# Performance work log

Measured on AMD Instinct MI355X. Metric: run time of the kernel, lower is better.

Reference implementation:

```python
import jax, jax.numpy as jnp
import numpy as np

N_HEADS = 16
N_KV_HEADS = 4
HEAD_DIM = 128
ROPE_THETA = 1000000.0

def setup_inputs() -> dict:
    key = jax.random.key(0)
    ks = jax.random.split(key, 5)
    B, T, D = 2, 2048, 2048
    s = 1.0 / np.sqrt(D)
    return {
        'x':  jax.random.normal(ks[0], (B, T, D), dtype=jnp.float32),
        'wq': jax.random.normal(ks[1], (D, N_HEADS * HEAD_DIM), dtype=jnp.float32) * s,
        'wk': jax.random.normal(ks[2], (D, N_KV_HEADS * HEAD_DIM), dtype=jnp.float32) * s,
        'wv': jax.random.normal(ks[3], (D, N_KV_HEADS * HEAD_DIM), dtype=jnp.float32) * s,
        'wo': jax.random.normal(ks[4], (N_HEADS * HEAD_DIM, D), dtype=jnp.float32) * s,
    }

def _rope_cos_sin(T, dtype):
    # build_rope_cache: inv_freq over half the head dim, cos/sin of shape [T, HEAD_DIM]
    half = HEAD_DIM // 2
    inv_freq = 1.0 / (ROPE_THETA ** (jnp.arange(0, half, dtype=jnp.float32) * 2.0 / HEAD_DIM))
    ang = jnp.arange(T, dtype=jnp.float32)[:, None] * inv_freq[None, :]  # [T, half]
    ang = jnp.concatenate([ang, ang], axis=-1)  # [T, HEAD_DIM]
    return jnp.cos(ang).astype(dtype), jnp.sin(ang).astype(dtype)

def _rotate_half(u):
    u1, u2 = jnp.split(u, 2, axis=-1)
    return jnp.concatenate([-u2, u1], axis=-1)

def _apply_rotary(h, cos, sin):
    # h: [B, H, T, hd]; cos/sin: [T, hd]
    return h * cos[None, None, :, :] + _rotate_half(h) * sin[None, None, :, :]

def _attention(x, wq, wk, wv, wo):
    B, T, D = x.shape
    dtype = x.dtype
    scale = HEAD_DIM ** -0.5
    # QKV projection + split heads -> [B, H, T, hd]
    qh = (x @ wq).reshape(B, T, N_HEADS, HEAD_DIM).transpose(0, 2, 1, 3)
    kh = (x @ wk).reshape(B, T, N_KV_HEADS, HEAD_DIM).transpose(0, 2, 1, 3)
    vh = (x @ wv).reshape(B, T, N_KV_HEADS, HEAD_DIM).transpose(0, 2, 1, 3)
    # RoPE
    cos, sin = _rope_cos_sin(T, dtype)
    qh = _apply_rotary(qh, cos, sin)
    kh = _apply_rotary(kh, cos, sin)
    # GQA: repeat kv heads
    rep = N_HEADS // N_KV_HEADS
    kh = jnp.repeat(kh, rep, axis=1)
    vh = jnp.repeat(vh, rep, axis=1)
    # eager attention: full score matrix [B, H, T, T]
    scores = jnp.einsum('bhtd,bhsd->bhts', qh, kh) * scale
    causal = jnp.tril(jnp.ones((T, T), dtype=bool))
    neg = jnp.asarray(jnp.finfo(jnp.float32).min, dtype=jnp.float32)
    scores = jnp.where(causal[None, None, :, :], scores.astype(jnp.float32), neg)
    probs = jax.nn.softmax(scores, axis=-1).astype(dtype)
    out = jnp.einsum('bhts,bhsd->bhtd', probs, vh)
    y = out.transpose(0, 2, 1, 3).reshape(B, T, N_HEADS * HEAD_DIM)  # merge heads
    return y @ wo

def reference(x, wq, wk, wv, wo):
    return _attention(x, wq, wk, wv, wo)
```

## Files before the change

kernel.cpp:

```cpp
#include <hip/hip_runtime.h>


#define T_SZ 2048
#define D_SZ 2048
#define BT   4096

typedef __attribute__((ext_vector_type(8))) short bf16x8;
typedef __attribute__((ext_vector_type(4))) float f32x4;

__device__ __forceinline__ unsigned short f2b(float f) {
  unsigned u = __float_as_uint(f);
  u = (u + 0x7fffu + ((u >> 16) & 1u)) >> 16;
  return (unsigned short)u;
}
__device__ __forceinline__ float b2f(unsigned short h) {
  return __uint_as_float(((unsigned)h) << 16);
}

#if __has_builtin(__builtin_amdgcn_exp2f)
__device__ __forceinline__ float exp2_fast(float x) { return __builtin_amdgcn_exp2f(x); }
#else
__device__ __forceinline__ float exp2_fast(float x) {
  float r; asm("v_exp_f32 %0, %1" : "=v"(r) : "v"(x)); return r;
}
#endif

__device__ __forceinline__ void async_ld16(const void* g, void* l) {
  __builtin_amdgcn_global_load_lds(
      (const __attribute__((address_space(1))) void*)g,
      (__attribute__((address_space(3))) void*)l, 16, 0, 0);
}

union Pack8 { unsigned short us[8]; uint4 v; };

__global__ __launch_bounds__(256) void prep(
    const float* __restrict__ x, unsigned short* __restrict__ xb,
    const float* __restrict__ wq, const float* __restrict__ wk,
    const float* __restrict__ wv, const float* __restrict__ wo,
    unsigned short* __restrict__ qkvT, unsigned short* __restrict__ woT) {
  __shared__ float tile[64][68];
  int bid = blockIdx.x, t = threadIdx.x;
  if (bid < 8192) {
    int i = (bid * 256 + t) * 4;
    float4 v = *(const float4*)(x + i);
    ushort4 o;
    o.x = f2b(v.x); o.y = f2b(v.y); o.z = f2b(v.z); o.w = f2b(v.w);
    *(ushort4*)(xb + i) = o;
    return;
  }
  int rem = bid - 8192;
  int bx = rem % 80, ky = rem / 80;
  const float* W; unsigned short* WT; int N, nb;
  if (bx < 32)      { W = wq; WT = qkvT;                       N = 2048; nb = bx; }
  else if (bx < 40) { W = wk; WT = qkvT + (size_t)2048 * 2048; N = 512;  nb = bx - 32; }
  else if (bx < 48) { W = wv; WT = qkvT + (size_t)2560 * 2048; N = 512;  nb = bx - 40; }
  else              { W = wo; WT = woT;                        N = 2048; nb = bx - 48; }
  const int K = 2048;
  int n0 = nb * 64, k0 = ky * 64;
#pragma unroll
  for (int i = 0; i < 4; i++) {
    int c = t + 256 * i;
    int r = c >> 4, cc = c & 15;
    float4 v = *(const float4*)(W + (size_t)(k0 + r) * N + n0 + cc * 4);
    tile[r][cc * 4 + 0] = v.x; tile[r][cc * 4 + 1] = v.y;
    tile[r][cc * 4 + 2] = v.z; tile[r][cc * 4 + 3] = v.w;
  }
  __syncthreads();
#pragma unroll
  for (int i = 0; i < 2; i++) {
    int c = t + 256 * i;
    int n = c >> 3, kc = c & 7;
    Pack8 p;
#pragma unroll
    for (int j = 0; j < 8; j++) p.us[j] = f2b(tile[kc * 8 + j][n]);
    *(uint4*)(WT + (size_t)(n0 + n) * K + k0 + kc * 8) = p.v;
  }
}

template <int OUT_BF16>
__global__ __launch_bounds__(256) void gemm_bt(
    const unsigned short* __restrict__ A, const unsigned short* __restrict__ Bt,
    void* __restrict__ C, int M, int N, int K) {
  __shared__ unsigned short As[2][128 * 32];
  __shared__ unsigned short Bs[2][128 * 32];
  int t = threadIdx.x;
  int lane = t & 63, wave = t >> 6;
  int lin = blockIdx.y * gridDim.x + blockIdx.x;
  int cpx = (gridDim.x * gridDim.y) >> 3;
  int swz = (lin & 7) * cpx + (lin >> 3);
  int bx = swz % gridDim.x, by = swz / gridDim.x;
  int m0 = by * 128, n0 = bx * 128;
  int wm = (wave >> 1) * 64, wn = (wave & 1) * 64;
  int fr = lane & 15, fq = lane >> 4;

  int srow = wave * 32 + (lane >> 2);
  int scol = (lane & 3) * 8;
  const unsigned short* Ag = A + (size_t)(m0 + srow) * K + scol;
  const unsigned short* Bg = Bt + (size_t)(n0 + srow) * K + scol;

  auto stage = [&](int k0_, int bf) {
#pragma unroll
    for (int j = 0; j < 2; j++) {
      async_ld16(Ag + (size_t)j * 16 * K + k0_, &As[bf][wave * 1024 + j * 512]);
      async_ld16(Bg + (size_t)j * 16 * K + k0_, &Bs[bf][wave * 1024 + j * 512]);
    }
  };

  f32x4 acc[4][4];
#pragma unroll
  for (int mi = 0; mi < 4; mi++)
#pragma unroll
    for (int ni = 0; ni < 4; ni++) acc[mi][ni] = (f32x4){0.f, 0.f, 0.f, 0.f};

  stage(0, 0);
  int cur = 0;
  for (int k0 = 0; k0 < K; k0 += 32) {
    if (k0 + 32 < K) {
      stage(k0 + 32, cur ^ 1);
      asm volatile("s_waitcnt vmcnt(4)" ::: "memory");
    } else {
      asm volatile("s_waitcnt vmcnt(0)" ::: "memory");
    }
    __builtin_amdgcn_s_barrier();
    asm volatile("" ::: "memory");
    bf16x8 a[4], b[4];
#pragma unroll
    for (int mi = 0; mi < 4; mi++)
      a[mi] = *(const bf16x8*)(&As[cur][(wm + 16 * mi + fr) * 32 + fq * 8]);
#pragma unroll
    for (int ni = 0; ni < 4; ni++)
      b[ni] = *(const bf16x8*)(&Bs[cur][(wn + 16 * ni + fr) * 32 + fq * 8]);
#pragma unroll
    for (int mi = 0; mi < 4; mi++)
#pragma unroll
      for (int ni = 0; ni < 4; ni++)
        acc[mi][ni] = __builtin_amdgcn_mfma_f32_16x16x32_bf16(
            a[mi], b[ni], acc[mi][ni], 0, 0, 0);
    asm volatile("s_waitcnt lgkmcnt(0)" ::: "memory");
    __builtin_amdgcn_s_barrier();
    asm volatile("" ::: "memory");
    cur ^= 1;
  }
#pragma unroll
  for (int mi = 0; mi < 4; mi++)
#pragma unroll
    for (int ni = 0; ni < 4; ni++)
#pragma unroll
      for (int r = 0; r < 4; r++) {
        int row = m0 + wm + 16 * mi + fq * 4 + r;
        int col = n0 + wn + 16 * ni + fr;
        float v = acc[mi][ni][r];
        if (OUT_BF16)
          ((unsigned short*)C)[(size_t)row * N + col] = f2b(v);
        else
          ((float*)C)[(size_t)row * N + col] = v;
      }
}

__global__ __launch_bounds__(256) void prep2(
    unsigned short* __restrict__ Kx ,
    const unsigned short* __restrict__ V ,
    unsigned short* __restrict__ VT) {
  __shared__ unsigned short tile[64][72];
  int bid = blockIdx.x, t = threadIdx.x;
  if (bid < 4096) {
    int p = bid * 256 + t;
    int d = p & 63;
    int h = (p >> 6) & 3;
    int row = p >> 8;
    int tpos = row & (T_SZ - 1);
    size_t base = (size_t)row * 3072 + h * 128 + d;
    float u1 = b2f(Kx[base]), u2 = b2f(Kx[base + 64]);
    float inv = expf(-(float)d * 0.21586735246819178f);
    float ang = (float)tpos * inv;
    float c = cosf(ang), s = sinf(ang);
    Kx[base]      = f2b(u1 * c - u2 * s);
    Kx[base + 64] = f2b(u2 * c + u1 * s);
    return;
  }
  int c0 = bid - 4096;
  int t0 = (c0 & 31) * 64;
  int n0 = ((c0 >> 5) & 1) * 64;
  int bk = c0 >> 6;
  int b = bk >> 2, kvh = bk & 3;
#pragma unroll
  for (int i = 0; i < 2; i++) {
    int c = t + 256 * i;
    int r = c >> 3, cc = c & 7;
    *(uint4*)&tile[r][cc * 8] = *(const uint4*)(
        V + (size_t)(b * T_SZ + t0 + r) * 3072 + kvh * 128 + n0 + cc * 8);
  }
  __syncthreads();
#pragma unroll
  for (int i = 0; i < 2; i++) {
    int c = t + 256 * i;
    int n = c >> 3, tc = c & 7;
    Pack8 p;
#pragma unroll
    for (int j = 0; j < 8; j++) p.us[j] = tile[tc * 8 + j][n];
    *(uint4*)(VT + ((size_t)bk * 128 + n0 + n) * T_SZ + t0 + tc * 8) = p.v;
  }
}

__global__ __launch_bounds__(512) void attn(
    const unsigned short* __restrict__ Q,
    const unsigned short* __restrict__ KV,
    const unsigned short* __restrict__ VT,
    unsigned short* __restrict__ O) {
  __shared__ unsigned short Ks[2][64 * 128];
  __shared__ unsigned short Vt[128 * 64];
  __shared__ unsigned short Ps[8][16 * 76];
  int qt = blockIdx.z ? blockIdx.x : 15 - blockIdx.x;
  int h = blockIdx.y, b = blockIdx.z;
  int kvh = h >> 2;
  int t = threadIdx.x, lane = t & 63, w = t >> 6;
  int fr = lane & 15, fq = lane >> 4;
  int rsw = fr & 7;

  bf16x8 qf[4];
#pragma unroll
  for (int kk = 0; kk < 4; kk++)
    qf[kk] = *(const bf16x8*)(
        Q + (size_t)(b * T_SZ + qt * 128 + w * 16 + fr) * 3072 +
        h * 128 + kk * 32 + fq * 8);

  const unsigned short* Kg = KV + (size_t)b * T_SZ * 3072 + kvh * 128;
  const unsigned short* Vg = VT + (size_t)(b * 4 + kvh) * 128 * T_SZ;

  int k_lr = lane >> 4, k_ls = lane & 15;
  int v_lr = lane >> 3, v_ls = lane & 7;

  auto stage_k = [&](int kt_, int bf) {
#pragma unroll
    for (int j = 0; j < 2; j++) {
      int row = w * 8 + j * 4 + k_lr;
      async_ld16(Kg + (size_t)(kt_ * 64 + row) * 3072 + ((k_ls ^ (row & 7)) << 3),
                 &Ks[bf][(w * 8 + j * 4) * 128]);
    }
  };
  auto stage_v = [&](int kt_) {
#pragma unroll
    for (int j = 0; j < 2; j++) {
      int row = w * 16 + j * 8 + v_lr;
      async_ld16(Vg + (size_t)row * T_SZ + kt_ * 64 + ((v_ls ^ (row & 7)) << 3),
                 &Vt[(w * 16 + j * 8) * 64]);
    }
  };

  stage_k(0, 0);
  stage_v(0);

  {
    const float QSCL = 0.08838834764831845f * 1.4426950408889634f;
    float tposf = (float)(qt * 128 + w * 16 + fr);
#pragma unroll
    for (int kk = 0; kk < 2; kk++)
#pragma unroll
      for (int j = 0; j < 8; j++) {
        int d = kk * 32 + (fq << 3) + j;
        float u1 = b2f((unsigned short)qf[kk][j]);
        float u2 = b2f((unsigned short)qf[kk + 2][j]);
        float inv = __expf(-(float)d * 0.21586735246819178f);
        float ang = tposf * inv, c, s;
        __sincosf(ang, &s, &c);
        qf[kk][j]     = (short)f2b((u1 * c - u2 * s) * QSCL);
        qf[kk + 2][j] = (short)f2b((u2 * c + u1 * s) * QSCL);
      }
  }

  f32x4 o[8];
#pragma unroll
  for (int i = 0; i < 8; i++) o[i] = (f32x4){0.f, 0.f, 0.f, 0.f};
  float mrow = -1e30f, lrow = 0.f;
  int qg = qt * 128 + w * 16 + fr;
  int nkt = 2 * qt + 2;

  int cur = 0;
  for (int kt = 0; kt < nkt; kt++) {
    if (kt + 1 < nkt) {
      stage_k(kt + 1, cur ^ 1);
      asm volatile("s_waitcnt vmcnt(2)" ::: "memory");
    } else {
      asm volatile("s_waitcnt vmcnt(0)" ::: "memory");
    }
    __builtin_amdgcn_s_barrier();
    asm volatile("" ::: "memory");

    const unsigned short* KsC = Ks[cur];

    f32x4 s[4];
    __builtin_amdgcn_s_setprio(1);
#pragma unroll
    for (int nn = 0; nn < 4; nn++) {
      s[nn] = (f32x4){0.f, 0.f, 0.f, 0.f};
#pragma unroll
      for (int kk = 0; kk < 4; kk++) {
        bf16x8 kf = *(const bf16x8*)(
            KsC + (nn * 16 + fr) * 128 + ((((kk << 2) + fq) ^ rsw) << 3));
        s[nn] = __builtin_amdgcn_mfma_f32_16x16x32_bf16(kf, qf[kk], s[nn], 0, 0, 0);
      }
    }
    __builtin_amdgcn_s_setprio(0);
    if (kt * 64 + 63 > qg) {
#pragma unroll
      for (int nn = 0; nn < 4; nn++)
#pragma unroll
        for (int r = 0; r < 4; r++) {
          int kvg = kt * 64 + nn * 16 + fq * 4 + r;
          if (kvg > qg) s[nn][r] = -1e30f;
        }
    }
    f32x4 t4;
#pragma unroll
    for (int r = 0; r < 4; r++)
      t4[r] = fmaxf(fmaxf(s[0][r], s[1][r]), fmaxf(s[2][r], s[3][r]));
    float mx = fmaxf(fmaxf(t4[0], t4[1]), fmaxf(t4[2], t4[3]));
    mx = fmaxf(mx, __shfl_xor(mx, 16, 64));
    mx = fmaxf(mx, __shfl_xor(mx, 32, 64));
    if (__any(mx > mrow + 8.0f)) {
      float mnew = fmaxf(mrow, mx);
      float alpha = exp2_fast(mrow - mnew);
      lrow *= alpha;
#pragma unroll
      for (int nt = 0; nt < 8; nt++)
#pragma unroll
        for (int r = 0; r < 4; r++) o[nt][r] *= alpha;
      mrow = mnew;
    }
    float sum = 0.f;
#pragma unroll
    for (int nn = 0; nn < 4; nn++) {
      ushort4 pk;
      float p0 = exp2_fast(s[nn][0] - mrow); pk.x = f2b(p0);
      float p1 = exp2_fast(s[nn][1] - mrow); pk.y = f2b(p1);
      float p2 = exp2_fast(s[nn][2] - mrow); pk.z = f2b(p2);
      float p3 = exp2_fast(s[nn][3] - mrow); pk.w = f2b(p3);
      sum += (p0 + p1) + (p2 + p3);
      *(ushort4*)(Ps[w] + fr * 76 + nn * 16 + fq * 4) = pk;
    }
    lrow += sum;
    __builtin_amdgcn_s_setprio(1);
#pragma unroll
    for (int kk = 0; kk < 2; kk++) {
      bf16x8 pf = *(const bf16x8*)(Ps[w] + fr * 76 + kk * 32 + fq * 8);
#pragma unroll
      for (int nt = 0; nt < 8; nt++) {
        bf16x8 vf = *(const bf16x8*)(
            Vt + (nt * 16 + fr) * 64 + ((((kk << 2) + fq) ^ rsw) << 3));
        o[nt] = __builtin_amdgcn_mfma_f32_16x16x32_bf16(vf, pf, o[nt], 0, 0, 0);
      }
    }
    __builtin_amdgcn_s_setprio(0);
    asm volatile("s_waitcnt lgkmcnt(0)" ::: "memory");
    __builtin_amdgcn_s_barrier();
    asm volatile("" ::: "memory");
    if (kt + 1 < nkt) stage_v(kt + 1);
    cur ^= 1;
  }
  float lsum = lrow;
  lsum += __shfl_xor(lsum, 16, 64);
  lsum += __shfl_xor(lsum, 32, 64);
  float linv = 1.f / lsum;
  int rowg = b * T_SZ + qt * 128 + w * 16 + fr;
#pragma unroll
  for (int nt = 0; nt < 8; nt++) {
    ushort4 ov;
    ov.x = f2b(o[nt][0] * linv);
    ov.y = f2b(o[nt][1] * linv);
    ov.z = f2b(o[nt][2] * linv);
    ov.w = f2b(o[nt][3] * linv);
    *(ushort4*)(O + (size_t)rowg * 2048 + h * 128 + nt * 16 + fq * 4) = ov;
  }
}

extern "C" void kernel_launch(void* const* d_in, const int* in_sizes, int n_in,
                              void* d_out, int out_size, void* d_ws, size_t ws_size,
                              hipStream_t stream) {
  const float* x  = (const float*)d_in[0];
  const float* wq = (const float*)d_in[1];
  const float* wk = (const float*)d_in[2];
  const float* wv = (const float*)d_in[3];
  const float* wo = (const float*)d_in[4];
  float* out = (float*)d_out;

  unsigned short* xb   = (unsigned short*)d_ws;
  unsigned short* wqT  = xb   + (size_t)4096 * 2048;
  unsigned short* woT  = wqT  + (size_t)3072 * 2048;
  unsigned short* QKVb = woT  + (size_t)2048 * 2048;
  unsigned short* VTb  = QKVb + (size_t)4096 * 3072;
  unsigned short* AOb  = VTb  + (size_t)4096 * 512;

  prep<<<10752, 256, 0, stream>>>(x, xb, wq, wk, wv, wo, wqT, woT);

  gemm_bt<1><<<dim3(24, 32), 256, 0, stream>>>(xb, wqT, QKVb, 4096, 3072, 2048);

  prep2<<<4608, 256, 0, stream>>>(QKVb + 2048, QKVb + 2560, VTb);

  attn<<<dim3(16, 16, 2), 512, 0, stream>>>(QKVb, QKVb + 2048, VTb, AOb);

  gemm_bt<0><<<dim3(16, 32), 256, 0, stream>>>(AOb, woT, (void*)out, 4096, 2048, 2048);
}
```

Measured before the change: 295.0 us.

## Fuse K RoPE and V transpose into QKV GEMM epilogue

Removes the separate prep2 kernel by handling K-head RoPE and the V transpose inside the QKV projection GEMM epilogue. Output tiles are staged through swizzled shared memory (the A/B buffers, now merged into one array, are reused). K tiles are rotated and written back, and V tiles are transposed into the VT layout. This saves one launch plus a global read and write pass over K and V. In exchange, those blocks carry a heavier, unbalanced epilogue with a scalar store loop and fast sincos approximations.

```diff
diff --git a/kernel.cpp b/kernel.cpp
--- a/kernel.cpp
+++ b/kernel.cpp
@@ -77,12 +77,12 @@
   }
 }
 
-template <int OUT_BF16>
+template <int MODE>
 __global__ __launch_bounds__(256) void gemm_bt(
     const unsigned short* __restrict__ A, const unsigned short* __restrict__ Bt,
-    void* __restrict__ C, int M, int N, int K) {
-  __shared__ unsigned short As[2][128 * 32];
-  __shared__ unsigned short Bs[2][128 * 32];
+    void* __restrict__ C, unsigned short* __restrict__ VT,
+    int M, int N, int K) {
+  __shared__ unsigned short smem[4][128 * 32];
   int t = threadIdx.x;
   int lane = t & 63, wave = t >> 6;
   int lin = blockIdx.y * gridDim.x + blockIdx.x;
@@ -101,8 +101,8 @@
   auto stage = [&](int k0_, int bf) {
 #pragma unroll
     for (int j = 0; j < 2; j++) {
-      async_ld16(Ag + (size_t)j * 16 * K + k0_, &As[bf][wave * 1024 + j * 512]);
-      async_ld16(Bg + (size_t)j * 16 * K + k0_, &Bs[bf][wave * 1024 + j * 512]);
+      async_ld16(Ag + (size_t)j * 16 * K + k0_, &smem[bf][wave * 1024 + j * 512]);
+      async_ld16(Bg + (size_t)j * 16 * K + k0_, &smem[2 + bf][wave * 1024 + j * 512]);
     }
   };
 
@@ -126,10 +126,10 @@
     bf16x8 a[4], b[4];
 #pragma unroll
     for (int mi = 0; mi < 4; mi++)
-      a[mi] = *(const bf16x8*)(&As[cur][(wm + 16 * mi + fr) * 32 + fq * 8]);
+      a[mi] = *(const bf16x8*)(&smem[cur][(wm + 16 * mi + fr) * 32 + fq * 8]);
 #pragma unroll
     for (int ni = 0; ni < 4; ni++)
-      b[ni] = *(const bf16x8*)(&Bs[cur][(wn + 16 * ni + fr) * 32 + fq * 8]);
+      b[ni] = *(const bf16x8*)(&smem[2 + cur][(wn + 16 * ni + fr) * 32 + fq * 8]);
 #pragma unroll
     for (int mi = 0; mi < 4; mi++)
 #pragma unroll
@@ -141,64 +141,79 @@
     asm volatile("" ::: "memory");
     cur ^= 1;
   }
+
+  if (MODE == 0) {
+#pragma unroll
+    for (int mi = 0; mi < 4; mi++)
+#pragma unroll
+      for (int ni = 0; ni < 4; ni++)
+#pragma unroll
+        for (int r = 0; r < 4; r++) {
+          int row = m0 + wm + 16 * mi + fq * 4 + r;
+          int col = n0 + wn + 16 * ni + fr;
+          ((float*)C)[(size_t)row * N + col] = acc[mi][ni][r];
+        }
+    return;
+  }
+
+  if (n0 < 2048) {
+#pragma unroll
+    for (int mi = 0; mi < 4; mi++)
+#pragma unroll
+      for (int ni = 0; ni < 4; ni++)
+#pragma unroll
+        for (int r = 0; r < 4; r++) {
+          int row = m0 + wm + 16 * mi + fq * 4 + r;
+          int col = n0 + wn + 16 * ni + fr;
+          ((unsigned short*)C)[(size_t)row * N + col] = f2b(acc[mi][ni][r]);
+        }
+    return;
+  }
+
+  unsigned short* Ex = &smem[0][0];
 #pragma unroll
   for (int mi = 0; mi < 4; mi++)
 #pragma unroll
     for (int ni = 0; ni < 4; ni++)
 #pragma unroll
       for (int r = 0; r < 4; r++) {
-        int row = m0 + wm + 16 * mi + fq * 4 + r;
-        int col = n0 + wn + 16 * ni + fr;
-        float v = acc[mi][ni][r];
-        if (OUT_BF16)
-          ((unsigned short*)C)[(size_t)row * N + col] = f2b(v);
-        else
-          ((float*)C)[(size_t)row * N + col] = v;
+        int row = wm + 16 * mi + fq * 4 + r;
+        int col = wn + 16 * ni + fr;
+        Ex[row * 128 + (col ^ ((row & 15) << 3))] = f2b(acc[mi][ni][r]);
       }
-}
-
-__global__ __launch_bounds__(256) void prep2(
-    unsigned short* __restrict__ Kx ,
-    const unsigned short* __restrict__ V ,
-    unsigned short* __restrict__ VT) {
-  __shared__ unsigned short tile[64][72];
-  int bid = blockIdx.x, t = threadIdx.x;
-  if (bid < 4096) {
-    int p = bid * 256 + t;
-    int d = p & 63;
-    int h = (p >> 6) & 3;
-    int row = p >> 8;
-    int tpos = row & (T_SZ - 1);
-    size_t base = (size_t)row * 3072 + h * 128 + d;
-    float u1 = b2f(Kx[base]), u2 = b2f(Kx[base + 64]);
-    float inv = expf(-(float)d * 0.21586735246819178f);
-    float ang = (float)tpos * inv;
-    float c = cosf(ang), s = sinf(ang);
-    Kx[base]      = f2b(u1 * c - u2 * s);
-    Kx[base + 64] = f2b(u2 * c + u1 * s);
-    return;
-  }
-  int c0 = bid - 4096;
-  int t0 = (c0 & 31) * 64;
-  int n0 = ((c0 >> 5) & 1) * 64;
-  int bk = c0 >> 6;
-  int b = bk >> 2, kvh = bk & 3;
-#pragma unroll
-  for (int i = 0; i < 2; i++) {
-    int c = t + 256 * i;
-    int r = c >> 3, cc = c & 7;
-    *(uint4*)&tile[r][cc * 8] = *(const uint4*)(
-        V + (size_t)(b * T_SZ + t0 + r) * 3072 + kvh * 128 + n0 + cc * 8);
-  }
   __syncthreads();
-#pragma unroll
-  for (int i = 0; i < 2; i++) {
-    int c = t + 256 * i;
-    int n = c >> 3, tc = c & 7;
-    Pack8 p;
-#pragma unroll
-    for (int j = 0; j < 8; j++) p.us[j] = tile[tc * 8 + j][n];
-    *(uint4*)(VT + ((size_t)bk * 128 + n0 + n) * T_SZ + t0 + tc * 8) = p.v;
+
+  if (n0 < 2560) {
+    for (int i = 0; i < 32; i++) {
+      int flat = t + 256 * i;
+      int row = flat >> 6;
+      int d = flat & 63;
+      int sw = (row & 15) << 3;
+      float u1 = b2f(Ex[row * 128 + (d ^ sw)]);
+      float u2 = b2f(Ex[row * 128 + ((d + 64) ^ sw)]);
+      int tpos = (m0 + row) & (T_SZ - 1);
+      float inv = __expf(-(float)d * 0.21586735246819178f);
+      float ang = (float)tpos * inv, cc, ss;
+      __sincosf(ang, &ss, &cc);
+      ((unsigned short*)C)[(size_t)(m0 + row) * N + n0 + d]      = f2b(u1 * cc - u2 * ss);
+      ((unsigned short*)C)[(size_t)(m0 + row) * N + n0 + d + 64] = f2b(u2 * cc + u1 * ss);
+    }
+  } else {
+    int kvh = (n0 - 2560) >> 7;
+    int bb = m0 >> 11, t0l = m0 & (T_SZ - 1);
+    int bk = bb * 4 + kvh;
+    for (int i = 0; i < 8; i++) {
+      int chunk = t + 256 * i;
+      int n = chunk >> 4;
+      int tc = chunk & 15;
+      Pack8 p;
+#pragma unroll
+      for (int j = 0; j < 8; j++) {
+        int tt = tc * 8 + j;
+        p.us[j] = Ex[tt * 128 + (n ^ ((tt & 15) << 3))];
+      }
+      *(uint4*)(VT + ((size_t)(bk * 128 + n)) * T_SZ + t0l + tc * 8) = p.v;
+    }
   }
 }
 
@@ -392,11 +407,10 @@
 
   prep<<<10752, 256, 0, stream>>>(x, xb, wq, wk, wv, wo, wqT, woT);
 
-  gemm_bt<1><<<dim3(24, 32), 256, 0, stream>>>(xb, wqT, QKVb, 4096, 3072, 2048);
-
-  prep2<<<4608, 256, 0, stream>>>(QKVb + 2048, QKVb + 2560, VTb);
+  gemm_bt<1><<<dim3(24, 32), 256, 0, stream>>>(xb, wqT, QKVb, VTb, 4096, 3072, 2048);
 
   attn<<<dim3(16, 16, 2), 512, 0, stream>>>(QKVb, QKVb + 2048, VTb, AOb);
 
-  gemm_bt<0><<<dim3(16, 32), 256, 0, stream>>>(AOb, woT, (void*)out, 4096, 2048, 2048);
-}
+  gemm_bt<0><<<dim3(16, 32), 256, 0, stream>>>(AOb, woT, (void*)out, nullptr,
+                                               4096, 2048, 2048);
+}
```

Result: faster. 288.5 us (-2.2%).
